# Optimization experiments

Hardware: AMD Instinct MI355X
Metric: run time of the kernel (lower is better)

## Reference

```python
import jax, jax.numpy as jnp
import numpy as np

ALIGNED_H, ALIGNED_W, ALIGNED_T = 7, 7, 4
SPATIAL_SCALE, TIME_SCALE = 1.0 / 16.0, 1.0
B, C, T, H, W = 4, 256, 16, 64, 64
N_ROIS = 1200


def setup_inputs() -> dict:
    key = jax.random.key(0)
    kf, kb, kx, ky, kw, kh, kt, kd = jax.random.split(key, 8)
    features = jax.random.normal(kf, (B, C, T, H, W), dtype=jnp.float32)
    b = jax.random.randint(kb, (N_ROIS,), 0, B).astype(jnp.float32)
    # image-space boxes (1024x1024 image, stride-16 features); temporal interval in frame units
    x1 = jax.random.uniform(kx, (N_ROIS,), minval=0.0, maxval=700.0)
    y1 = jax.random.uniform(ky, (N_ROIS,), minval=0.0, maxval=700.0)
    x2 = jnp.minimum(x1 + jax.random.uniform(kw, (N_ROIS,), minval=32.0, maxval=320.0), 1023.0)
    y2 = jnp.minimum(y1 + jax.random.uniform(kh, (N_ROIS,), minval=32.0, maxval=320.0), 1023.0)
    t1 = jax.random.uniform(kt, (N_ROIS,), minval=0.0, maxval=10.0)
    t2 = jnp.minimum(t1 + jax.random.uniform(kd, (N_ROIS,), minval=2.0, maxval=6.0), 15.0)
    rois = jnp.stack([b, x1, y1, x2, y2, t1, t2], axis=1)  # [N, 7]
    return {"features": features, "rois": rois}


def _axis_samples(start, end, size, n_out):
    # classic roi_align sampling: bin = (end - start + 1) / (n_out - 1), sample at start + i*bin
    length = jnp.maximum(end - start + 1.0, 1.0)                                  # [N]
    step = length / (n_out - 1.0)
    coord = start[:, None] + step[:, None] * jnp.arange(n_out, dtype=jnp.float32)[None, :]  # [N, n_out]
    valid = (coord >= 0.0) & (coord < size)
    lo = jnp.clip(jnp.floor(coord), 0.0, size - 1.0)
    frac = coord - lo
    lo_i = lo.astype(jnp.int32)
    hi_i = jnp.minimum(lo_i + 1, size - 1)
    return lo_i, hi_i, frac, valid.astype(jnp.float32)


def roi_align_3d(features, rois, p_t, p_h, p_w, sscale, tscale):
    Bf, Cf, Tf, Hf, Wf = features.shape
    f = jnp.transpose(features, (0, 2, 3, 4, 1))  # [B,T,H,W,C] channel-last for clean gather
    bidx = rois[:, 0].astype(jnp.int32)
    x1 = rois[:, 1] * sscale
    y1 = rois[:, 2] * sscale
    x2 = rois[:, 3] * sscale
    y2 = rois[:, 4] * sscale
    t1 = rois[:, 5] * tscale
    t2 = rois[:, 6] * tscale
    tl, th, tfr, tv = _axis_samples(t1, t2, Tf, p_t)  # [N, p_t]
    yl, yh, yfr, yv = _axis_samples(y1, y2, Hf, p_h)  # [N, p_h]
    xl, xh, xfr, xv = _axis_samples(x1, x2, Wf, p_w)  # [N, p_w]
    b4 = bidx[:, None, None, None]
    out = jnp.zeros((rois.shape[0], p_t, p_h, p_w, Cf), dtype=features.dtype)
    # trilinear interpolation: sum over 8 corners
    for ti, wt in ((tl, 1.0 - tfr), (th, tfr)):
        for yi, wy in ((yl, 1.0 - yfr), (yh, yfr)):
            for xi, wx in ((xl, 1.0 - xfr), (xh, xfr)):
                v = f[b4, ti[:, :, None, None], yi[:, None, :, None], xi[:, None, None, :]]  # [N,pt,ph,pw,C]
                w = wt[:, :, None, None] * wy[:, None, :, None] * wx[:, None, None, :]
                out = out + v * w[..., None]
    # zero out-of-bounds sample points (matches CUDA kernel behavior)
    mask = tv[:, :, None, None] * yv[:, None, :, None] * xv[:, None, None, :]
    out = out * mask[..., None]
    return jnp.transpose(out, (0, 4, 1, 2, 3))  # [N, C, p_t, p_h, p_w]


def _avg_pool3d_k2s1(x):
    s = x[..., :-1, :, :] + x[..., 1:, :, :]
    s = s[..., :, :-1, :] + s[..., :, 1:, :]
    s = s[..., :, :, :-1] + s[..., :, :, 1:]
    return s * 0.125


def reference(features, rois):
    x = roi_align_3d(features, rois, ALIGNED_T + 1, ALIGNED_H + 1, ALIGNED_W + 1,
                     SPATIAL_SCALE, TIME_SCALE)
    return _avg_pool3d_k2s1(x)  # [N, C, ALIGNED_T, ALIGNED_H, ALIGNED_W]
```

## Files before the change

### kernel.cpp

```cpp
#include <hip/hip_runtime.h>

#define C_ 256
#define T_ 16
#define H_ 64
#define W_ 64
#define PT 5
#define PH 8
#define PW 8
#define OT 4
#define OH 7
#define OW 7
#define SSCALE (1.0f/16.0f)
#define TSCALE 1.0f
#define CG 32
#define LROW 66
#define PLN (CG * LROW)
#define NOUT (CG * OT * OH * OW)

typedef float f4v __attribute__((ext_vector_type(4)));
typedef float f2v __attribute__((ext_vector_type(2)));
typedef _Float16 h2v __attribute__((ext_vector_type(2)));
typedef _Float16 h8v __attribute__((ext_vector_type(8)));

__device__ __forceinline__ f4v lo4(h8v h) {
    f4v r = {(float)h[0], (float)h[1], (float)h[2], (float)h[3]};
    return r;
}
__device__ __forceinline__ f4v hi4(h8v h) {
    f4v r = {(float)h[4], (float)h[5], (float)h[6], (float)h[7]};
    return r;
}

__global__ __launch_bounds__(256) void transpose_kernel(const float* __restrict__ f,
                                                        _Float16* __restrict__ ft) {
    __shared__ unsigned tile[64 * 128];
    const int THW = T_ * H_ * W_;
    int thw0 = blockIdx.x * 64;
    int b = blockIdx.y;
    int q = threadIdx.x & 15;
    int cp0 = threadIdx.x >> 4;

#pragma unroll
    for (int k = 0; k < 8; ++k) {
        int cp = k * 16 + cp0;
        int c = cp * 2;
        const f4v* s0 = reinterpret_cast<const f4v*>(
            &f[((size_t)b * C_ + c) * THW + thw0 + q * 4]);
        const f4v* s1 = reinterpret_cast<const f4v*>(
            &f[((size_t)b * C_ + c + 1) * THW + thw0 + q * 4]);
        f4v va = __builtin_nontemporal_load(s0);
        f4v vb = __builtin_nontemporal_load(s1);
#pragma unroll
        for (int j = 0; j < 4; ++j) {
            int row = q * 4 + j;
            h2v hp = {(_Float16)va[j], (_Float16)vb[j]};
            tile[row * 128 + (cp ^ (row & 30))] = __builtin_bit_cast(unsigned, hp);
        }
    }
    __syncthreads();

    int wv = threadIdx.x >> 6;
    int ln = threadIdx.x & 63;
    size_t orow = ((size_t)b * THW + thw0) * C_;
#pragma unroll
    for (int i = 0; i < 16; ++i) {
        int row = wv * 16 + i;
        int s = row & 30;
        uint2 w = *reinterpret_cast<const uint2*>(&tile[row * 128 + ((ln * 2) ^ s)]);
        *reinterpret_cast<uint2*>(&ft[orow + (size_t)row * C_ + ln * 4]) = w;
    }
}

__global__ __launch_bounds__(1024) void sort_rois(const float* __restrict__ rois,
                                                  int nroi, int* __restrict__ perm) {
    __shared__ unsigned key[2048];
    int t = threadIdx.x;
    if (nroi > 2048) {
        for (int i = t; i < nroi; i += 1024) perm[i] = i;
        return;
    }
    for (int i = t; i < 2048; i += 1024) {
        unsigned k = 0x1FFFFFu;
        if (i < nroi) {
            const float* rp = rois + i * 7;
            int bb = (int)rp[0];
            float xc = (rp[1] + rp[3]) * 0.5f * SSCALE;
            float yc = (rp[2] + rp[4]) * 0.5f * SSCALE;
            float tc = (rp[5] + rp[6]) * 0.5f * TSCALE;
            int xq = min(63, max(0, (int)xc));
            int yq = min(63, max(0, (int)yc));
            int tq = min(15, max(0, (int)tc));
            unsigned m = 0;
#pragma unroll
            for (int bit = 0; bit < 6; ++bit)
                m |= (((yq >> bit) & 1u) << (2 * bit + 1)) |
                     (((xq >> bit) & 1u) << (2 * bit));
            k = ((((unsigned)bb << 12) | m) << 4) | (unsigned)tq;
        }
        key[i] = (k << 11) | (unsigned)i;
    }
    __syncthreads();
    for (int kk = 2; kk <= 2048; kk <<= 1) {
        for (int j = kk >> 1; j > 0; j >>= 1) {
            for (int i = t; i < 2048; i += 1024) {
                int ixj = i ^ j;
                if (ixj > i) {
                    unsigned a = key[i], c = key[ixj];
                    bool up = (i & kk) == 0;
                    if ((a > c) == up) { key[i] = c; key[ixj] = a; }
                }
            }
            __syncthreads();
        }
    }
    for (int i = t; i < 2048; i += 1024)
        if (i < nroi) perm[i] = (int)(key[i] & 0x7FFu);
}

__global__ __launch_bounds__(256, 4) void roi_kernel(const _Float16* __restrict__ ft,
                                                     const float* __restrict__ rois,
                                                     const int* __restrict__ perm,
                                                     float* __restrict__ out) {
    __shared__ float scratch[NOUT];
    __shared__ float sroi[7];
    __shared__ int2 s_trow[PT]; __shared__ float2 s_twt[PT];
    __shared__ int2 s_yrow[PH]; __shared__ float2 s_ywt[PH];
    __shared__ int2 s_xoff[PW]; __shared__ float2 s_xwt[PW];

    int bid = blockIdx.x;
    int r = perm[bid >> 3];
    int cg = bid & 7;
    int c0 = cg * CG;

    if (threadIdx.x < 7) sroi[threadIdx.x] = rois[r * 7 + threadIdx.x];
    __syncthreads();

    if (threadIdx.x < 21) {
        int i = threadIdx.x;
        float start, end, size;
        int j, n, scale;
        if (i < 5) {
            j = i; n = PT;
            start = sroi[5] * TSCALE; end = sroi[6] * TSCALE;
            size = (float)T_; scale = H_ * W_ * C_ * 2;
        } else if (i < 13) {
            j = i - 5; n = PH;
            start = sroi[2] * SSCALE; end = sroi[4] * SSCALE;
            size = (float)H_; scale = W_ * C_ * 2;
        } else {
            j = i - 13; n = PW;
            start = sroi[1] * SSCALE; end = sroi[3] * SSCALE;
            size = (float)W_; scale = C_ * 2;
        }
        float length = fmaxf(end - start + 1.0f, 1.0f);
        float step = length / (float)(n - 1);
        float coord = start + step * (float)j;
        float valid = (coord >= 0.0f && coord < size) ? 1.0f : 0.0f;
        float lo = fminf(fmaxf(floorf(coord), 0.0f), size - 1.0f);
        int lo_i = (int)lo;
        int hi_i = min(lo_i + 1, (int)size - 1);
        float fr = coord - lo;
        int2 offs; offs.x = lo_i * scale; offs.y = hi_i * scale;
        float2 wts; wts.x = (1.0f - fr) * valid; wts.y = fr * valid;
        if (i < 5)       { s_trow[j] = offs; s_twt[j] = wts; }
        else if (i < 13) { s_yrow[j] = offs; s_ywt[j] = wts; }
        else             { s_xoff[j] = offs; s_xwt[j] = wts; }
    }
    __syncthreads();

    int b = (int)sroi[0];
    int c4 = threadIdx.x & 3;
    int slot = threadIdx.x >> 2;
    const char* fb = (const char*)ft
        + ((size_t)b * (T_ * H_ * W_ * C_) + (size_t)(c0 + c4 * 8)) * 2;

    float* bufs[2] = {scratch, scratch + PLN};
    int cc = threadIdx.x & 31;
    int hh = threadIdx.x >> 5;

    float racc[OT][OW];
#pragma unroll
    for (int t = 0; t < OT; ++t)
#pragma unroll
        for (int w = 0; w < OW; ++w) racc[t][w] = 0.0f;

    int y = slot >> 3, x = slot & 7;
    int2 yr = s_yrow[y]; float2 yw = s_ywt[y];
    int2 xo = s_xoff[x]; float2 xw = s_xwt[x];
    int o00 = yr.x + xo.x, o01 = yr.x + xo.y;
    int o10 = yr.y + xo.x, o11 = yr.y + xo.y;

    h8v cur[8], nxt[8];
    {
        int2 tr = s_trow[0];
        cur[0] = *(const h8v*)(fb + tr.x + o00);
        cur[1] = *(const h8v*)(fb + tr.x + o01);
        cur[2] = *(const h8v*)(fb + tr.x + o10);
        cur[3] = *(const h8v*)(fb + tr.x + o11);
        cur[4] = *(const h8v*)(fb + tr.y + o00);
        cur[5] = *(const h8v*)(fb + tr.y + o01);
        cur[6] = *(const h8v*)(fb + tr.y + o10);
        cur[7] = *(const h8v*)(fb + tr.y + o11);
    }

#pragma unroll
    for (int t = 0; t < PT; ++t) {
        if (t + 1 < PT) {
            int2 tr = s_trow[t + 1];
            nxt[0] = *(const h8v*)(fb + tr.x + o00);
            nxt[1] = *(const h8v*)(fb + tr.x + o01);
            nxt[2] = *(const h8v*)(fb + tr.x + o10);
            nxt[3] = *(const h8v*)(fb + tr.x + o11);
            nxt[4] = *(const h8v*)(fb + tr.y + o00);
            nxt[5] = *(const h8v*)(fb + tr.y + o01);
            nxt[6] = *(const h8v*)(fb + tr.y + o10);
            nxt[7] = *(const h8v*)(fb + tr.y + o11);
        }

        float2 tw = s_twt[t];
        f4v vx00L = xw.x * lo4(cur[0]) + xw.y * lo4(cur[1]);
        f4v vx01L = xw.x * lo4(cur[2]) + xw.y * lo4(cur[3]);
        f4v vx10L = xw.x * lo4(cur[4]) + xw.y * lo4(cur[5]);
        f4v vx11L = xw.x * lo4(cur[6]) + xw.y * lo4(cur[7]);
        f4v vx00H = xw.x * hi4(cur[0]) + xw.y * hi4(cur[1]);
        f4v vx01H = xw.x * hi4(cur[2]) + xw.y * hi4(cur[3]);
        f4v vx10H = xw.x * hi4(cur[4]) + xw.y * hi4(cur[5]);
        f4v vx11H = xw.x * hi4(cur[6]) + xw.y * hi4(cur[7]);
        f4v vL = tw.x * (yw.x * vx00L + yw.y * vx01L)
               + tw.y * (yw.x * vx10L + yw.y * vx11L);
        f4v vH = tw.x * (yw.x * vx00H + yw.y * vx01H)
               + tw.y * (yw.x * vx10H + yw.y * vx11H);

        float* bp = bufs[t & 1];
        {
            float* col = &bp[(c4 * 8) * LROW + slot];
            col[0 * LROW] = vL[0];
            col[1 * LROW] = vL[1];
            col[2 * LROW] = vL[2];
            col[3 * LROW] = vL[3];
            col[4 * LROW] = vH[0];
            col[5 * LROW] = vH[1];
            col[6 * LROW] = vH[2];
            col[7 * LROW] = vH[3];
        }
        __syncthreads();

        if (hh < 7) {
            const float* p = &bp[cc * LROW + hh * 8];
            float p2[8];
#pragma unroll
            for (int x2 = 0; x2 < 4; ++x2) {
                f2v a = *(const f2v*)(p + 2 * x2);
                f2v bq = *(const f2v*)(p + 8 + 2 * x2);
                f2v s = a + bq;
                p2[2 * x2] = s[0];
                p2[2 * x2 + 1] = s[1];
            }
#pragma unroll
            for (int w = 0; w < OW; ++w) {
                float pw = p2[w] + p2[w + 1];
                if (t < OT) racc[t][w] += pw;
                if (t > 0) racc[t - 1][w] += pw;
            }
        }

#pragma unroll
        for (int i = 0; i < 8; ++i) cur[i] = nxt[i];
    }
    __syncthreads();

    if (hh < 7) {
        int base = cc * (OT * OH * OW) + hh * OW;
#pragma unroll
        for (int t = 0; t < OT; ++t)
#pragma unroll
            for (int w = 0; w < OW; ++w)
                scratch[base + t * (OH * OW) + w] = racc[t][w] * 0.125f;
    }
    __syncthreads();

    float* outb = out + ((size_t)r * C_ + c0) * (OT * OH * OW);
    const f4v* s4 = (const f4v*)scratch;
    f4v* o4 = (f4v*)outb;
    for (int k = 0; k < 7; ++k) {
        int idx = k * 256 + threadIdx.x;
        if (idx < NOUT / 4) __builtin_nontemporal_store(s4[idx], &o4[idx]);
    }
}

__device__ __forceinline__ void axis_sample(float start, float end, float size, int n,
                                            int j, int& lo_i, int& hi_i, float& frac,
                                            float& valid) {
    float length = fmaxf(end - start + 1.0f, 1.0f);
    float step = length / (float)(n - 1);
    float coord = start + step * (float)j;
    valid = (coord >= 0.0f && coord < size) ? 1.0f : 0.0f;
    float lo = fminf(fmaxf(floorf(coord), 0.0f), size - 1.0f);
    frac = coord - lo;
    lo_i = (int)lo;
    hi_i = min(lo_i + 1, (int)size - 1);
}

__global__ void roi_direct(const float* __restrict__ f, const float* __restrict__ rois,
                           float* __restrict__ out, long long total) {
    long long idx = (long long)blockIdx.x * 256 + threadIdx.x;
    if (idx >= total) return;
    int w = (int)(idx % OW);
    long long q = idx / OW;
    int h = (int)(q % OH);
    q /= OH;
    int t = (int)(q % OT);
    q /= OT;
    int c = (int)(q % C_);
    int r = (int)(q / C_);

    float rb = rois[r * 7 + 0];
    float x1 = rois[r * 7 + 1] * SSCALE;
    float y1 = rois[r * 7 + 2] * SSCALE;
    float x2 = rois[r * 7 + 3] * SSCALE;
    float y2 = rois[r * 7 + 4] * SSCALE;
    float t1 = rois[r * 7 + 5] * TSCALE;
    float t2 = rois[r * 7 + 6] * TSCALE;
    int b = (int)rb;
    const float* fc = f + ((size_t)b * C_ + c) * (T_ * H_ * W_);

    float acc = 0.0f;
    for (int dt = 0; dt < 2; ++dt) {
        int tlo, thi; float tf, tv;
        axis_sample(t1, t2, (float)T_, PT, t + dt, tlo, thi, tf, tv);
        for (int dh = 0; dh < 2; ++dh) {
            int ylo, yhi; float yf, yv;
            axis_sample(y1, y2, (float)H_, PH, h + dh, ylo, yhi, yf, yv);
            for (int dw = 0; dw < 2; ++dw) {
                int xlo, xhi; float xf, xv;
                axis_sample(x1, x2, (float)W_, PW, w + dw, xlo, xhi, xf, xv);
                float v000 = fc[(tlo * H_ + ylo) * W_ + xlo];
                float v001 = fc[(tlo * H_ + ylo) * W_ + xhi];
                float v010 = fc[(tlo * H_ + yhi) * W_ + xlo];
                float v011 = fc[(tlo * H_ + yhi) * W_ + xhi];
                float v100 = fc[(thi * H_ + ylo) * W_ + xlo];
                float v101 = fc[(thi * H_ + ylo) * W_ + xhi];
                float v110 = fc[(thi * H_ + yhi) * W_ + xlo];
                float v111 = fc[(thi * H_ + yhi) * W_ + xhi];
                float vx00 = v000 + xf * (v001 - v000);
                float vx01 = v010 + xf * (v011 - v010);
                float vx10 = v100 + xf * (v101 - v100);
                float vx11 = v110 + xf * (v111 - v110);
                float vy0 = vx00 + yf * (vx01 - vx00);
                float vy1 = vx10 + yf * (vx11 - vx10);
                float v = vy0 + tf * (vy1 - vy0);
                acc += v * (tv * yv * xv);
            }
        }
    }
    out[idx] = acc * 0.125f;
}

extern "C" void kernel_launch(void* const* d_in, const int* in_sizes, int n_in,
                              void* d_out, int out_size, void* d_ws, size_t ws_size,
                              hipStream_t stream) {
    const float* feat = (const float*)d_in[0];
    const float* rois = (const float*)d_in[1];
    float* out = (float*)d_out;
    int nroi = in_sizes[1] / 7;
    int B = in_sizes[0] / (C_ * T_ * H_ * W_);
    size_t ftbytes = (size_t)B * T_ * H_ * W_ * C_ * sizeof(_Float16);
    size_t need = ftbytes + 2048 * sizeof(int);

    if (ws_size >= need && nroi >= 1) {
        _Float16* ft = (_Float16*)d_ws;
        int* perm = (int*)((char*)d_ws + ftbytes);
        sort_rois<<<1, 1024, 0, stream>>>(rois, nroi, perm);
        dim3 g1(T_ * H_ * W_ / 64, B);
        transpose_kernel<<<g1, 256, 0, stream>>>(feat, ft);
        roi_kernel<<<dim3(nroi * (C_ / CG)), 256, 0, stream>>>(ft, rois, perm, out);
    } else {
        long long total = (long long)nroi * C_ * OT * OH * OW;
        roi_direct<<<(int)((total + 255) / 256), 256, 0, stream>>>(feat, rois, out, total);
    }
}
```

Measured before the change: 524.2 us.

## Widen ROI blocks to 64 channels with 512 threads, drop register prefetch

Each block now handles 64 channels instead of 32, using 512 threads, so there are half as many blocks per ROI and the per-ROI setup (ROI load, axis sampling, syncs) is amortized over more channels. The explicit next-timestep register double-buffering of the eight h8v loads is removed in favor of loading inside the loop, which lowers register pressure. The cost is less latency hiding within each thread, larger shared-memory scratch per block, and fewer resident blocks. The launch-bounds occupancy hint is also removed.

```diff
diff --git a/kernel.cpp b/kernel.cpp
--- a/kernel.cpp
+++ b/kernel.cpp
@@ -12,7 +12,7 @@
 #define OW 7
 #define SSCALE (1.0f/16.0f)
 #define TSCALE 1.0f
-#define CG 32
+#define CG 64
 #define LROW 66
 #define PLN (CG * LROW)
 #define NOUT (CG * OT * OH * OW)
@@ -117,10 +117,10 @@
         if (i < nroi) perm[i] = (int)(key[i] & 0x7FFu);
 }
 
-__global__ __launch_bounds__(256, 4) void roi_kernel(const _Float16* __restrict__ ft,
-                                                     const float* __restrict__ rois,
-                                                     const int* __restrict__ perm,
-                                                     float* __restrict__ out) {
+__global__ __launch_bounds__(512) void roi_kernel(const _Float16* __restrict__ ft,
+                                                  const float* __restrict__ rois,
+                                                  const int* __restrict__ perm,
+                                                  float* __restrict__ out) {
     __shared__ float scratch[NOUT];
     __shared__ float sroi[7];
     __shared__ int2 s_trow[PT]; __shared__ float2 s_twt[PT];
@@ -128,8 +128,8 @@
     __shared__ int2 s_xoff[PW]; __shared__ float2 s_xwt[PW];
 
     int bid = blockIdx.x;
-    int r = perm[bid >> 3];
-    int cg = bid & 7;
+    int r = perm[bid >> 2];
+    int cg = bid & 3;
     int c0 = cg * CG;
 
     if (threadIdx.x < 7) sroi[threadIdx.x] = rois[r * 7 + threadIdx.x];
@@ -169,14 +169,14 @@
     __syncthreads();
 
     int b = (int)sroi[0];
-    int c4 = threadIdx.x & 3;
-    int slot = threadIdx.x >> 2;
+    int c8 = threadIdx.x & 7;
+    int slot = threadIdx.x >> 3;
     const char* fb = (const char*)ft
-        + ((size_t)b * (T_ * H_ * W_ * C_) + (size_t)(c0 + c4 * 8)) * 2;
+        + ((size_t)b * (T_ * H_ * W_ * C_) + (size_t)(c0 + c8 * 8)) * 2;
 
     float* bufs[2] = {scratch, scratch + PLN};
-    int cc = threadIdx.x & 31;
-    int hh = threadIdx.x >> 5;
+    int cc = threadIdx.x & 63;
+    int hh = threadIdx.x >> 6;
 
     float racc[OT][OW];
 #pragma unroll
@@ -190,42 +190,27 @@
     int o00 = yr.x + xo.x, o01 = yr.x + xo.y;
     int o10 = yr.y + xo.x, o11 = yr.y + xo.y;
 
-    h8v cur[8], nxt[8];
-    {
-        int2 tr = s_trow[0];
-        cur[0] = *(const h8v*)(fb + tr.x + o00);
-        cur[1] = *(const h8v*)(fb + tr.x + o01);
-        cur[2] = *(const h8v*)(fb + tr.x + o10);
-        cur[3] = *(const h8v*)(fb + tr.x + o11);
-        cur[4] = *(const h8v*)(fb + tr.y + o00);
-        cur[5] = *(const h8v*)(fb + tr.y + o01);
-        cur[6] = *(const h8v*)(fb + tr.y + o10);
-        cur[7] = *(const h8v*)(fb + tr.y + o11);
-    }
-
 #pragma unroll
     for (int t = 0; t < PT; ++t) {
-        if (t + 1 < PT) {
-            int2 tr = s_trow[t + 1];
-            nxt[0] = *(const h8v*)(fb + tr.x + o00);
-            nxt[1] = *(const h8v*)(fb + tr.x + o01);
-            nxt[2] = *(const h8v*)(fb + tr.x + o10);
-            nxt[3] = *(const h8v*)(fb + tr.x + o11);
-            nxt[4] = *(const h8v*)(fb + tr.y + o00);
-            nxt[5] = *(const h8v*)(fb + tr.y + o01);
-            nxt[6] = *(const h8v*)(fb + tr.y + o10);
-            nxt[7] = *(const h8v*)(fb + tr.y + o11);
-        }
-
+        int2 tr = s_trow[t];
         float2 tw = s_twt[t];
-        f4v vx00L = xw.x * lo4(cur[0]) + xw.y * lo4(cur[1]);
-        f4v vx01L = xw.x * lo4(cur[2]) + xw.y * lo4(cur[3]);
-        f4v vx10L = xw.x * lo4(cur[4]) + xw.y * lo4(cur[5]);
-        f4v vx11L = xw.x * lo4(cur[6]) + xw.y * lo4(cur[7]);
-        f4v vx00H = xw.x * hi4(cur[0]) + xw.y * hi4(cur[1]);
-        f4v vx01H = xw.x * hi4(cur[2]) + xw.y * hi4(cur[3]);
-        f4v vx10H = xw.x * hi4(cur[4]) + xw.y * hi4(cur[5]);
-        f4v vx11H = xw.x * hi4(cur[6]) + xw.y * hi4(cur[7]);
+        h8v q00 = *(const h8v*)(fb + tr.x + o00);
+        h8v q01 = *(const h8v*)(fb + tr.x + o01);
+        h8v q10 = *(const h8v*)(fb + tr.x + o10);
+        h8v q11 = *(const h8v*)(fb + tr.x + o11);
+        h8v p00 = *(const h8v*)(fb + tr.y + o00);
+        h8v p01 = *(const h8v*)(fb + tr.y + o01);
+        h8v p10 = *(const h8v*)(fb + tr.y + o10);
+        h8v p11 = *(const h8v*)(fb + tr.y + o11);
+
+        f4v vx00L = xw.x * lo4(q00) + xw.y * lo4(q01);
+        f4v vx01L = xw.x * lo4(q10) + xw.y * lo4(q11);
+        f4v vx10L = xw.x * lo4(p00) + xw.y * lo4(p01);
+        f4v vx11L = xw.x * lo4(p10) + xw.y * lo4(p11);
+        f4v vx00H = xw.x * hi4(q00) + xw.y * hi4(q01);
+        f4v vx01H = xw.x * hi4(q10) + xw.y * hi4(q11);
+        f4v vx10H = xw.x * hi4(p00) + xw.y * hi4(p01);
+        f4v vx11H = xw.x * hi4(p10) + xw.y * hi4(p11);
         f4v vL = tw.x * (yw.x * vx00L + yw.y * vx01L)
                + tw.y * (yw.x * vx10L + yw.y * vx11L);
         f4v vH = tw.x * (yw.x * vx00H + yw.y * vx01H)
@@ -233,7 +218,7 @@
 
         float* bp = bufs[t & 1];
         {
-            float* col = &bp[(c4 * 8) * LROW + slot];
+            float* col = &bp[(c8 * 8) * LROW + slot];
             col[0 * LROW] = vL[0];
             col[1 * LROW] = vL[1];
             col[2 * LROW] = vL[2];
@@ -263,9 +248,6 @@
                 if (t > 0) racc[t - 1][w] += pw;
             }
         }
-
-#pragma unroll
-        for (int i = 0; i < 8; ++i) cur[i] = nxt[i];
     }
     __syncthreads();
 
@@ -282,8 +264,9 @@
     float* outb = out + ((size_t)r * C_ + c0) * (OT * OH * OW);
     const f4v* s4 = (const f4v*)scratch;
     f4v* o4 = (f4v*)outb;
+#pragma unroll
     for (int k = 0; k < 7; ++k) {
-        int idx = k * 256 + threadIdx.x;
+        int idx = k * 512 + threadIdx.x;
         if (idx < NOUT / 4) __builtin_nontemporal_store(s4[idx], &o4[idx]);
     }
 }
@@ -373,7 +356,7 @@
         sort_rois<<<1, 1024, 0, stream>>>(rois, nroi, perm);
         dim3 g1(T_ * H_ * W_ / 64, B);
         transpose_kernel<<<g1, 256, 0, stream>>>(feat, ft);
-        roi_kernel<<<dim3(nroi * (C_ / CG)), 256, 0, stream>>>(ft, rois, perm, out);
+        roi_kernel<<<dim3(nroi * (C_ / CG)), 512, 0, stream>>>(ft, rois, perm, out);
     } else {
         long long total = (long long)nroi * C_ * OT * OH * OW;
         roi_direct<<<(int)((total + 255) / 256), 256, 0, stream>>>(feat, rois, out, total);
```

After: 524.2 us. Within noise of the previous version (-0.0%).
